# Kernel optimization log

Measured on AMD Instinct MI355X. Metric: run time of the kernel, lower is better.

The kernel has to match this reference:

```python
import jax, jax.numpy as jnp
import numpy as np

EPS = 0.1           # entropic regularization epsilon
MAX_ITER = 100
THRESH = 0.1        # early-stop threshold on mean |u - u_prev|
LOG_EPS = 1e-8


def setup_inputs() -> dict:
    key = jax.random.key(0)
    kx, ky = jax.random.split(key)
    x = jax.random.normal(kx, (8, 1024, 3), dtype=jnp.float32)
    y = jax.random.normal(ky, (8, 1024, 3), dtype=jnp.float32)
    return {"x": x, "y": y}


def _sqdist(x, y):
    # squared euclidean cost matrix [B, N, N]  (== torch.cdist(x,y,p=2)**2)
    x2 = jnp.sum(x * x, axis=-1)[:, :, None]
    y2 = jnp.sum(y * y, axis=-1)[:, None, :]
    xy = jnp.einsum("bnd,bmd->bnm", x, y)
    return jnp.maximum(x2 + y2 - 2.0 * xy, 0.0)


def reference(x, y):
    B, N, D = x.shape
    C = _sqdist(x, y)                      # [B, N, N]
    log_mu = jnp.log(1.0 / N + LOG_EPS)    # scalar (uniform marginals)
    log_nu = log_mu

    u0 = jnp.zeros((B, N), dtype=x.dtype)
    v0 = jnp.zeros((B, N), dtype=x.dtype)

    def step(carry, _):
        u, v, done = carry
        # u-update uses old v
        M1 = (u[:, :, None] + v[:, None, :] - C) / EPS          # [B,N,N]
        u_new = EPS * (log_mu - jax.nn.logsumexp(M1, axis=-1)) + u
        # v-update uses new u
        M2 = (u_new[:, :, None] + v[:, None, :] - C) / EPS
        v_new = EPS * (log_nu - jax.nn.logsumexp(M2, axis=-2)) + v
        # freeze once converged (mimics torch early break)
        u_out = jnp.where(done, u, u_new)
        v_out = jnp.where(done, v, v_new)
        err = jnp.mean(jnp.abs(u_out - u))
        done_new = done | (err < THRESH)
        return (u_out, v_out, done_new), None

    (u, v, _), _ = jax.lax.scan(step, (u0, v0, jnp.array(False)), None, length=MAX_ITER)

    PI = jnp.exp((u[:, :, None] + v[:, None, :] - C) / EPS)     # transport plan
    emd = jnp.sum(PI * C, axis=(-2, -1))                        # [B]
    return jnp.mean(emd)                                        # reduction='mean'
```

## Files before the change

kernel.cpp:

```cpp
#include <hip/hip_runtime.h>

typedef unsigned int uint_t;

constexpr int B = 8;
constexpr int N = 1024;
constexpr int NBLOCKS = 256;
constexpr int NTHREADS = 512;
constexpr int NWAVES = NTHREADS / 64;
constexpr int BPB = NBLOCKS / B;
constexpr int SEG = N / BPB;
constexpr int RPW = SEG / NWAVES;
constexpr int KPL = N / 64;
constexpr int MAX_ITER = 100;
constexpr float THRESH = 0.1f;
constexpr float K2 = 14.42695040888963f;
constexpr float A2K = 2.0f * K2;
constexpr float NEPSLN2 = -0.06931471805599453f;
constexpr float EPSLOGMU = -0.693146156565634f;
constexpr uint_t MAGIC = 0xC0FFEE01u;

constexpr int OFF_U      = 0;
constexpr int OFF_V      = OFF_U + B * N;
constexpr int OFF_ERRBLK = OFF_V + B * N;
constexpr int OFF_ERRBAT = OFF_ERRBLK + 256;
constexpr int OFF_EMDBLK = OFF_ERRBAT + 800;
constexpr int OFF_EMDBAT = OFF_EMDBLK + 256;
constexpr int OFF_ZERO   = OFF_EMDBAT + 8;
constexpr int OFF_BARFLG = OFF_ZERO;
constexpr int OFF_ERRFLG = OFF_BARFLG + 256;
constexpr int OFF_EMDFLG = OFF_ERRFLG + 8;
constexpr int OFF_ZEROEND= OFF_EMDFLG + 8;
constexpr int OFF_INIT   = OFF_ZEROEND;

__device__ __forceinline__ float gload(const float* p) {
  return __hip_atomic_load(p, __ATOMIC_RELAXED, __HIP_MEMORY_SCOPE_AGENT);
}
__device__ __forceinline__ void gstore(float* p, float v) {
  __hip_atomic_store(p, v, __ATOMIC_RELAXED, __HIP_MEMORY_SCOPE_AGENT);
}
__device__ __forceinline__ uint_t lflag(const uint_t* p) {
  return __hip_atomic_load(p, __ATOMIC_RELAXED, __HIP_MEMORY_SCOPE_AGENT);
}
__device__ __forceinline__ void sflag_rel(uint_t* p, uint_t v) {
  __hip_atomic_store(p, v, __ATOMIC_RELEASE, __HIP_MEMORY_SCOPE_AGENT);
}

__device__ __forceinline__ float wsum(float v) {
#pragma unroll
  for (int o = 32; o; o >>= 1) v += __shfl_xor(v, o);
  return v;
}
__device__ __forceinline__ float wmax(float v) {
#pragma unroll
  for (int o = 32; o; o >>= 1) v = fmaxf(v, __shfl_xor(v, o));
  return v;
}

__device__ __forceinline__ float block_sum(float v, float* sh) {
  v = wsum(v);
  const int wave = threadIdx.x >> 6;
  const int lane = threadIdx.x & 63;
  if (lane == 0) sh[wave] = v;
  __syncthreads();
  float tot = 0.f;
#pragma unroll
  for (int w = 0; w < NWAVES; ++w) tot += sh[w];
  __syncthreads();
  return tot;
}

__device__ __forceinline__ void batch_barrier(uint_t* flg, int seg, uint_t epoch,
                                              int lane) {
  __syncthreads();
  if (threadIdx.x == 0) sflag_rel(&flg[seg], epoch);
  if (threadIdx.x < 64) {
    for (;;) {
      uint_t f = (lane < BPB) ? lflag(&flg[lane]) : epoch;
      if (__all(f >= epoch)) break;
      __builtin_amdgcn_s_sleep(1);
    }
  }
  __syncthreads();
}

template <bool TRACK>
__device__ __forceinline__ float half_update(
    const float4 (&c)[KPL], const float4* __restrict__ s_row,
    const float* __restrict__ pin, float* __restrict__ pout,
    int seg, int wave, int lane, bool pin_zero, bool first_out) {
  float p2[KPL];
#pragma unroll
  for (int k = 0; k < KPL; ++k)
    p2[k] = pin_zero ? 0.f : gload(&pin[lane + (k << 6)]) * K2;

  float err = 0.f;
#pragma unroll
  for (int rr = 0; rr < RPW; ++rr) {
    const int i = seg * SEG + wave * RPW + rr;
    float4 r4 = s_row[i];
    float a0 = A2K * r4.x, a1 = A2K * r4.y, a2 = A2K * r4.z;
    float X = -r4.w;
    float vals[KPL];
    float m = -3.4e38f;
#pragma unroll
    for (int k = 0; k < KPL; ++k) {
      float t = fmaf(a0, c[k].x, fmaf(a1, c[k].y, fmaf(a2, c[k].z, c[k].w)));
      float val = fminf(t - X, 0.f) + p2[k];
      vals[k] = val;
      m = fmaxf(m, val);
    }
    m = wmax(m);
    float s = 0.f;
#pragma unroll
    for (int k = 0; k < KPL; ++k)
      s += __builtin_amdgcn_exp2f(vals[k] - m);
    s = wsum(s);
    float pnew = fmaf(NEPSLN2, m + __builtin_amdgcn_logf(s), EPSLOGMU);
    if (lane == 0) {
      if (TRACK) err += fabsf(pnew - (first_out ? 0.f : gload(&pout[i])));
      gstore(&pout[i], pnew);
    }
  }
  return err;
}

__global__ void __launch_bounds__(NTHREADS, 2) sinkhorn_kernel(
    const float* __restrict__ xg, const float* __restrict__ yg,
    float* __restrict__ out, float* __restrict__ ws) {
  __shared__ float4 s_x4[N];
  __shared__ float4 s_y4[N];
  __shared__ float sh_red[NWAVES];

  const int bid = blockIdx.x;
  const int tid = threadIdx.x;
  const int b = bid & 7;
  const int seg = bid >> 3;
  const int wave = tid >> 6;
  const int lane = tid & 63;

  float* u = ws + OFF_U + b * N;
  float* v = ws + OFF_V + b * N;
  float* err_blk = ws + OFF_ERRBLK + b * 32;
  float* err_bat = ws + OFF_ERRBAT;
  float* emd_blk = ws + OFF_EMDBLK + b * 32;
  float* emd_bat = ws + OFF_EMDBAT;
  uint_t* bar_flg = (uint_t*)(ws + OFF_BARFLG) + b * 32;
  uint_t* err_flg = (uint_t*)(ws + OFF_ERRFLG);
  uint_t* emd_flg = (uint_t*)(ws + OFF_EMDFLG);
  uint_t* init_flag = (uint_t*)(ws + OFF_INIT);

  for (int p = tid; p < N; p += NTHREADS) {
    const float* xp = xg + (size_t)(b * N + p) * 3;
    float x0 = xp[0], x1 = xp[1], x2 = xp[2];
    s_x4[p] = make_float4(x0, x1, x2, -K2 * (x0 * x0 + x1 * x1 + x2 * x2));
    const float* yp = yg + (size_t)(b * N + p) * 3;
    float y0 = yp[0], y1 = yp[1], y2 = yp[2];
    s_y4[p] = make_float4(y0, y1, y2, -K2 * (y0 * y0 + y1 * y1 + y2 * y2));
  }
  __syncthreads();

  float4 cY[KPL], cX[KPL];
#pragma unroll
  for (int k = 0; k < KPL; ++k) {
    cY[k] = s_y4[lane + (k << 6)];
    cX[k] = s_x4[lane + (k << 6)];
  }

  if (bid == 0) {
    uint_t* zb = (uint_t*)(ws + OFF_ZERO);
    for (int i = tid; i < OFF_ZEROEND - OFF_ZERO; i += NTHREADS)
      __hip_atomic_store(&zb[i], 0u, __ATOMIC_RELAXED, __HIP_MEMORY_SCOPE_AGENT);
    __syncthreads();
    if (tid == 0) sflag_rel(init_flag, MAGIC);
  } else if (tid == 0) {
    while (lflag(init_flag) != MAGIC) __builtin_amdgcn_s_sleep(2);
  }
  __syncthreads();

  uint_t epoch = 0;
  for (int it = 0; it < MAX_ITER; ++it) {
    float my_err = half_update<true>(cY, s_x4, v, u, seg, wave, lane,
                                     it == 0, it == 0);
    float blk_err = block_sum(my_err, sh_red);
    if (tid == 0) gstore(&err_blk[seg], blk_err);
    ++epoch;
    batch_barrier(bar_flg, seg, epoch, lane);

    if (seg == 0 && tid == 0) {
      float s = 0.f;
      for (int q = 0; q < BPB; ++q) s += gload(&err_blk[q]);
      gstore(&err_bat[it * B + b], s);
      sflag_rel(&err_flg[b], (uint_t)(it + 1));
    }

    half_update<false>(cX, s_y4, u, v, seg, wave, lane, false, false);
    ++epoch;
    batch_barrier(bar_flg, seg, epoch, lane);

    if (tid < 64) {
      const uint_t want = (uint_t)(it + 1);
      for (;;) {
        uint_t f = (lane < B) ? lflag(&err_flg[lane]) : want;
        if (__all(f >= want)) break;
        __builtin_amdgcn_s_sleep(1);
      }
      float e = (lane < B) ? gload(&err_bat[it * B + lane]) : 0.f;
      e = wsum(e);
      if (lane == 0) sh_red[0] = e;
    }
    __syncthreads();
    float tot = sh_red[0];
    __syncthreads();
    if (tot * (1.f / (B * N)) < THRESH) break;
  }

  float p2[KPL];
#pragma unroll
  for (int k = 0; k < KPL; ++k) p2[k] = gload(&v[lane + (k << 6)]) * K2;
  float acc = 0.f;
#pragma unroll
  for (int rr = 0; rr < RPW; ++rr) {
    const int i = seg * SEG + wave * RPW + rr;
    float4 r4 = s_x4[i];
    float a0 = A2K * r4.x, a1 = A2K * r4.y, a2 = A2K * r4.z;
    float X = -r4.w;
    float u2 = gload(&u[i]) * K2;
#pragma unroll
    for (int k = 0; k < KPL; ++k) {
      float t = fmaf(a0, cY[k].x, fmaf(a1, cY[k].y, fmaf(a2, cY[k].z, cY[k].w)));
      float kc = fmaxf(X - t, 0.f);
      acc = fmaf(__builtin_amdgcn_exp2f(u2 + p2[k] - kc), kc, acc);
    }
  }
  float blk = block_sum(acc, sh_red);
  if (tid == 0) gstore(&emd_blk[seg], blk);
  ++epoch;
  batch_barrier(bar_flg, seg, epoch, lane);
  if (seg == 0 && tid == 0) {
    float s = 0.f;
    for (int q = 0; q < BPB; ++q) s += gload(&emd_blk[q]);
    gstore(&emd_bat[b], s);
    sflag_rel(&emd_flg[b], 1u);
  }
  if (bid == 0 && tid < 64) {
    for (;;) {
      uint_t f = (lane < B) ? lflag(&emd_flg[lane]) : 1u;
      if (__all(f >= 1u)) break;
      __builtin_amdgcn_s_sleep(1);
    }
    float e = (lane < B) ? gload(&emd_bat[lane]) : 0.f;
    e = wsum(e);
    if (lane == 0) out[0] = e * (1.f / (B * K2));
  }
}

extern "C" void kernel_launch(void* const* d_in, const int* in_sizes, int n_in,
                              void* d_out, int out_size, void* d_ws, size_t ws_size,
                              hipStream_t stream) {
  const float* x = (const float*)d_in[0];
  const float* y = (const float*)d_in[1];
  float* out = (float*)d_out;
  float* ws = (float*)d_ws;
  void* args[] = { (void*)&x, (void*)&y, (void*)&out, (void*)&ws };
  hipLaunchCooperativeKernel((const void*)sinkhorn_kernel,
                             dim3(NBLOCKS), dim3(NTHREADS), args, 0, stream);
}
```

Before: 133.3 us.

## Double threads per block, batch rows per wave, overlap u-update with convergence wait

Raises the block size to 1024 threads so each wave handles fewer rows. Rows are processed in a batch per k-column, reading SoA column data from LDS instead of register-cached float4. The next u-update is computed speculatively before waiting for the global convergence check, and its store is deferred until after the check, which hides the cross-batch flag wait. It also replaces the final EMD barrier with a one-sided flag wait, and moves input loading ahead of the init wait. The trade-off is more LDS reads and a possibly wasted u computation on the last iteration.

New measurement: 138.5 us. +3.9%, slower.

```diff
diff --git a/kernel.cpp b/kernel.cpp
--- a/kernel.cpp
+++ b/kernel.cpp
@@ -5,7 +5,7 @@
 constexpr int B = 8;
 constexpr int N = 1024;
 constexpr int NBLOCKS = 256;
-constexpr int NTHREADS = 512;
+constexpr int NTHREADS = 1024;
 constexpr int NWAVES = NTHREADS / 64;
 constexpr int BPB = NBLOCKS / B;
 constexpr int SEG = N / BPB;
@@ -84,51 +84,72 @@
 }
 
 template <bool TRACK>
-__device__ __forceinline__ float half_update(
-    const float4 (&c)[KPL], const float4* __restrict__ s_row,
-    const float* __restrict__ pin, float* __restrict__ pout,
-    int seg, int wave, int lane, bool pin_zero, bool first_out) {
+__device__ __forceinline__ float half_compute(
+    const float* __restrict__ cx, const float* __restrict__ cy,
+    const float* __restrict__ cz, const float* __restrict__ cw,
+    const float* __restrict__ rx, const float* __restrict__ ry,
+    const float* __restrict__ rz, const float* __restrict__ rw,
+    const float* __restrict__ pin, const float* __restrict__ pout_old,
+    float (&pnew)[RPW], int i0, int lane, bool pin_zero, bool first_out) {
   float p2[KPL];
 #pragma unroll
   for (int k = 0; k < KPL; ++k)
     p2[k] = pin_zero ? 0.f : gload(&pin[lane + (k << 6)]) * K2;
 
+  float a0[RPW], a1[RPW], a2[RPW], X[RPW], m[RPW];
+  float vals[RPW][KPL];
+#pragma unroll
+  for (int rr = 0; rr < RPW; ++rr) {
+    a0[rr] = A2K * rx[i0 + rr]; a1[rr] = A2K * ry[i0 + rr];
+    a2[rr] = A2K * rz[i0 + rr];
+    X[rr] = -rw[i0 + rr];
+    m[rr] = -3.4e38f;
+  }
+#pragma unroll
+  for (int k = 0; k < KPL; ++k) {
+    const int j = lane + (k << 6);
+    float ccx = cx[j], ccy = cy[j], ccz = cz[j];
+    float base = cw[j] + p2[k];
+#pragma unroll
+    for (int rr = 0; rr < RPW; ++rr) {
+      float t = fmaf(a0[rr], ccx, fmaf(a1[rr], ccy, fmaf(a2[rr], ccz, base)));
+      float val = fminf(t - X[rr], p2[k]);
+      vals[rr][k] = val;
+      m[rr] = fmaxf(m[rr], val);
+    }
+  }
   float err = 0.f;
 #pragma unroll
   for (int rr = 0; rr < RPW; ++rr) {
-    const int i = seg * SEG + wave * RPW + rr;
-    float4 r4 = s_row[i];
-    float a0 = A2K * r4.x, a1 = A2K * r4.y, a2 = A2K * r4.z;
-    float X = -r4.w;
-    float vals[KPL];
-    float m = -3.4e38f;
-#pragma unroll
-    for (int k = 0; k < KPL; ++k) {
-      float t = fmaf(a0, c[k].x, fmaf(a1, c[k].y, fmaf(a2, c[k].z, c[k].w)));
-      float val = fminf(t - X, 0.f) + p2[k];
-      vals[k] = val;
-      m = fmaxf(m, val);
-    }
-    m = wmax(m);
+    float mr = wmax(m[rr]);
     float s = 0.f;
 #pragma unroll
     for (int k = 0; k < KPL; ++k)
-      s += __builtin_amdgcn_exp2f(vals[k] - m);
+      s += __builtin_amdgcn_exp2f(vals[rr][k] - mr);
     s = wsum(s);
-    float pnew = fmaf(NEPSLN2, m + __builtin_amdgcn_logf(s), EPSLOGMU);
-    if (lane == 0) {
-      if (TRACK) err += fabsf(pnew - (first_out ? 0.f : gload(&pout[i])));
-      gstore(&pout[i], pnew);
+    float pn = fmaf(NEPSLN2, mr + __builtin_amdgcn_logf(s), EPSLOGMU);
+    pnew[rr] = pn;
+    if (TRACK && lane == 0) {
+      float old = first_out ? 0.f : gload(&pout_old[i0 + rr]);
+      err += fabsf(pn - old);
     }
   }
   return err;
 }
 
-__global__ void __launch_bounds__(NTHREADS, 2) sinkhorn_kernel(
+__device__ __forceinline__ void store_rows(float* p, const float (&pnew)[RPW],
+                                           int i0, int lane) {
+  if (lane == 0) {
+#pragma unroll
+    for (int rr = 0; rr < RPW; ++rr) gstore(&p[i0 + rr], pnew[rr]);
+  }
+}
+
+__global__ void __launch_bounds__(NTHREADS) sinkhorn_kernel(
     const float* __restrict__ xg, const float* __restrict__ yg,
     float* __restrict__ out, float* __restrict__ ws) {
-  __shared__ float4 s_x4[N];
-  __shared__ float4 s_y4[N];
+  __shared__ float s_xx[N], s_xy[N], s_xz[N], s_xw[N];
+  __shared__ float s_yx[N], s_yy[N], s_yz[N], s_yw[N];
   __shared__ float sh_red[NWAVES];
 
   const int bid = blockIdx.x;
@@ -137,6 +158,7 @@
   const int seg = bid >> 3;
   const int wave = tid >> 6;
   const int lane = tid & 63;
+  const int i0 = seg * SEG + wave * RPW;
 
   float* u = ws + OFF_U + b * N;
   float* v = ws + OFF_V + b * N;
@@ -149,53 +171,67 @@
   uint_t* emd_flg = (uint_t*)(ws + OFF_EMDFLG);
   uint_t* init_flag = (uint_t*)(ws + OFF_INIT);
 
-  for (int p = tid; p < N; p += NTHREADS) {
-    const float* xp = xg + (size_t)(b * N + p) * 3;
-    float x0 = xp[0], x1 = xp[1], x2 = xp[2];
-    s_x4[p] = make_float4(x0, x1, x2, -K2 * (x0 * x0 + x1 * x1 + x2 * x2));
-    const float* yp = yg + (size_t)(b * N + p) * 3;
-    float y0 = yp[0], y1 = yp[1], y2 = yp[2];
-    s_y4[p] = make_float4(y0, y1, y2, -K2 * (y0 * y0 + y1 * y1 + y2 * y2));
-  }
-  __syncthreads();
-
-  float4 cY[KPL], cX[KPL];
-#pragma unroll
-  for (int k = 0; k < KPL; ++k) {
-    cY[k] = s_y4[lane + (k << 6)];
-    cX[k] = s_x4[lane + (k << 6)];
-  }
-
   if (bid == 0) {
     uint_t* zb = (uint_t*)(ws + OFF_ZERO);
     for (int i = tid; i < OFF_ZEROEND - OFF_ZERO; i += NTHREADS)
       __hip_atomic_store(&zb[i], 0u, __ATOMIC_RELAXED, __HIP_MEMORY_SCOPE_AGENT);
     __syncthreads();
     if (tid == 0) sflag_rel(init_flag, MAGIC);
-  } else if (tid == 0) {
+  }
+
+  for (int p = tid; p < N; p += NTHREADS) {
+    const float* xp = xg + (size_t)(b * N + p) * 3;
+    float x0 = xp[0], x1 = xp[1], x2 = xp[2];
+    s_xx[p] = x0; s_xy[p] = x1; s_xz[p] = x2;
+    s_xw[p] = -K2 * (x0 * x0 + x1 * x1 + x2 * x2);
+    const float* yp = yg + (size_t)(b * N + p) * 3;
+    float y0 = yp[0], y1 = yp[1], y2 = yp[2];
+    s_yx[p] = y0; s_yy[p] = y1; s_yz[p] = y2;
+    s_yw[p] = -K2 * (y0 * y0 + y1 * y1 + y2 * y2);
+  }
+  __syncthreads();
+
+  float un[RPW];
+  float my_err = half_compute<true>(s_yx, s_yy, s_yz, s_yw,
+                                    s_xx, s_xy, s_xz, s_xw,
+                                    v, u, un, i0, lane,
+                                    true, true);
+  store_rows(u, un, i0, lane);
+  float blk_err = block_sum(my_err, sh_red);
+  if (tid == 0) gstore(&err_blk[seg], blk_err);
+
+  if (tid == 0 && bid != 0)
     while (lflag(init_flag) != MAGIC) __builtin_amdgcn_s_sleep(2);
-  }
   __syncthreads();
 
   uint_t epoch = 0;
-  for (int it = 0; it < MAX_ITER; ++it) {
-    float my_err = half_update<true>(cY, s_x4, v, u, seg, wave, lane,
-                                     it == 0, it == 0);
-    float blk_err = block_sum(my_err, sh_red);
-    if (tid == 0) gstore(&err_blk[seg], blk_err);
+  int it = 0;
+  for (;;) {
     ++epoch;
     batch_barrier(bar_flg, seg, epoch, lane);
 
-    if (seg == 0 && tid == 0) {
-      float s = 0.f;
-      for (int q = 0; q < BPB; ++q) s += gload(&err_blk[q]);
-      gstore(&err_bat[it * B + b], s);
-      sflag_rel(&err_flg[b], (uint_t)(it + 1));
-    }
-
-    half_update<false>(cX, s_y4, u, v, seg, wave, lane, false, false);
+    float vn[RPW];
+    half_compute<false>(s_xx, s_xy, s_xz, s_xw,
+                        s_yx, s_yy, s_yz, s_yw,
+                        u, nullptr, vn, i0, lane, false, false);
+    store_rows(v, vn, i0, lane);
+
+    if (seg == 0 && tid < 64) {
+      float e = (lane < BPB) ? gload(&err_blk[lane]) : 0.f;
+      e = wsum(e);
+      if (lane == 0) {
+        gstore(&err_bat[it * B + b], e);
+        sflag_rel(&err_flg[b], (uint_t)(it + 1));
+      }
+    }
     ++epoch;
     batch_barrier(bar_flg, seg, epoch, lane);
+
+    if (it == MAX_ITER - 1) break;
+
+    my_err = half_compute<true>(s_yx, s_yy, s_yz, s_yw,
+                                s_xx, s_xy, s_xz, s_xw,
+                                v, u, un, i0, lane, false, false);
 
     if (tid < 64) {
       const uint_t want = (uint_t)(it + 1);
@@ -212,35 +248,44 @@
     float tot = sh_red[0];
     __syncthreads();
     if (tot * (1.f / (B * N)) < THRESH) break;
-  }
-
-  float p2[KPL];
-#pragma unroll
-  for (int k = 0; k < KPL; ++k) p2[k] = gload(&v[lane + (k << 6)]) * K2;
+
+    store_rows(u, un, i0, lane);
+    blk_err = block_sum(my_err, sh_red);
+    if (tid == 0) gstore(&err_blk[seg], blk_err);
+    ++it;
+  }
+
+  float p2e[KPL];
+#pragma unroll
+  for (int k = 0; k < KPL; ++k) p2e[k] = gload(&v[lane + (k << 6)]) * K2;
   float acc = 0.f;
 #pragma unroll
   for (int rr = 0; rr < RPW; ++rr) {
-    const int i = seg * SEG + wave * RPW + rr;
-    float4 r4 = s_x4[i];
-    float a0 = A2K * r4.x, a1 = A2K * r4.y, a2 = A2K * r4.z;
-    float X = -r4.w;
+    const int i = i0 + rr;
+    float a0 = A2K * s_xx[i], a1 = A2K * s_xy[i], a2 = A2K * s_xz[i];
+    float X = -s_xw[i];
     float u2 = gload(&u[i]) * K2;
 #pragma unroll
     for (int k = 0; k < KPL; ++k) {
-      float t = fmaf(a0, cY[k].x, fmaf(a1, cY[k].y, fmaf(a2, cY[k].z, cY[k].w)));
+      const int j = lane + (k << 6);
+      float t = fmaf(a0, s_yx[j], fmaf(a1, s_yy[j], fmaf(a2, s_yz[j], s_yw[j])));
       float kc = fmaxf(X - t, 0.f);
-      acc = fmaf(__builtin_amdgcn_exp2f(u2 + p2[k] - kc), kc, acc);
+      acc = fmaf(__builtin_amdgcn_exp2f(u2 + p2e[k] - kc), kc, acc);
     }
   }
   float blk = block_sum(acc, sh_red);
-  if (tid == 0) gstore(&emd_blk[seg], blk);
-  ++epoch;
-  batch_barrier(bar_flg, seg, epoch, lane);
-  if (seg == 0 && tid == 0) {
-    float s = 0.f;
-    for (int q = 0; q < BPB; ++q) s += gload(&emd_blk[q]);
-    gstore(&emd_bat[b], s);
-    sflag_rel(&emd_flg[b], 1u);
+  const uint_t ef = epoch + 1;
+  if (tid == 0) { gstore(&emd_blk[seg], blk); sflag_rel(&bar_flg[seg], ef); }
+
+  if (seg == 0 && tid < 64) {
+    for (;;) {
+      uint_t f = (lane < BPB) ? lflag(&bar_flg[lane]) : ef;
+      if (__all(f >= ef)) break;
+      __builtin_amdgcn_s_sleep(1);
+    }
+    float e = (lane < BPB) ? gload(&emd_blk[lane]) : 0.f;
+    e = wsum(e);
+    if (lane == 0) { gstore(&emd_bat[b], e); sflag_rel(&emd_flg[b], 1u); }
   }
   if (bid == 0 && tid < 64) {
     for (;;) {
```
